# Optimization experiments

Hardware: AMD Instinct MI355X
Metric: run time of the kernel (lower is better)

## Reference

```python
import jax, jax.numpy as jnp
import numpy as np


def _component_indices(d, j):
    # Butterfly component at level j has block size k = d >> j.
    k = d >> j
    half = k // 2
    base = np.arange(d // k) * k                       # block starts
    p = (base[:, None] + np.arange(half)[None, :]).reshape(-1)  # [d//2]
    q = p + half
    return p, q


def butterfly_rotation(thetas, d):
    """Compose m = log2(d) butterfly components: R = B(d,d) @ B(d,d/2) @ ... @ B(d,2).
    thetas: [m, d//2] Givens angles per component (block-major order as in torch)."""
    m = thetas.shape[0]
    R = jnp.eye(d, dtype=thetas.dtype)
    for j in range(m):
        p, q = _component_indices(d, j)
        c = jnp.cos(thetas[j])
        s = jnp.sin(thetas[j])
        C = jnp.eye(d, dtype=thetas.dtype)
        C = C.at[p, p].set(c)
        C = C.at[q, q].set(c)
        C = C.at[p, q].set(-s)
        C = C.at[q, p].set(s)
        R = R @ C
    return R


def setup_inputs() -> dict:
    key = jax.random.key(0)
    ks = jax.random.split(key, 8)
    N, D_IN, D_OUT, R = 16384, 4096, 4096, 1024
    M = 10  # log2(R)
    return {
        "x": jax.random.normal(ks[0], (N, D_IN), dtype=jnp.float32),
        "W": jax.random.normal(ks[1], (D_OUT, D_IN), dtype=jnp.float32) * 0.02,
        "bias": jax.random.normal(ks[2], (D_OUT,), dtype=jnp.float32) * 0.02,
        "U": jax.random.normal(ks[3], (D_OUT, R), dtype=jnp.float32) * 0.02,
        "S": jax.random.uniform(ks[4], (R,), dtype=jnp.float32),
        "V": jax.random.normal(ks[5], (R, D_IN), dtype=jnp.float32) * 0.02,
        "thetas_u": jax.random.normal(ks[6], (M, R // 2), dtype=jnp.float32) * 0.1,
        "thetas_v": jax.random.normal(ks[7], (M, R // 2), dtype=jnp.float32) * 0.1,
    }


def reference(x, W, bias, U, S, V, thetas_u, thetas_v):
    r = S.shape[0]
    R_U = butterfly_rotation(thetas_u, r)  # [r, r]
    R_V = butterfly_rotation(thetas_v, r)  # [r, r]
    # base_layer(x)
    base = x @ W.T + bias                  # [N, out]
    # adapter: x @ V^T @ R_V @ diag(S) @ R_U^T @ U^T
    h = (x @ V.T) @ R_V                    # [N, r]
    h = h * S                              # diag(S)
    delta = (h @ R_U.T) @ U.T              # [N, out]
    return base + delta
```

## Files before the change

kernel.cpp:

```cpp
#include <hip/hip_runtime.h>
#include <cstdint>
#include <cstddef>


typedef __bf16 bf16x8 __attribute__((ext_vector_type(8)));
typedef float floatx4 __attribute__((ext_vector_type(4)));
typedef unsigned short ushortx8 __attribute__((ext_vector_type(8)));

__device__ __forceinline__ unsigned short f2bf(float f) {
    unsigned int u = __builtin_bit_cast(unsigned int, f);
    u += 0x7FFFu + ((u >> 16) & 1u);
    return (unsigned short)(u >> 16);
}

__device__ __forceinline__ void gld_lds16(const void* g, void* l) {
    __builtin_amdgcn_global_load_lds(
        (const __attribute__((address_space(1))) void*)g,
        (__attribute__((address_space(3))) void*)l,
        16, 0, 0);
}

__global__ __launch_bounds__(256) void butterfly_rows_kernel(
    const float* __restrict__ thetas_v, const float* __restrict__ thetas_u,
    const float* __restrict__ S,
    unsigned short* __restrict__ RVsb, unsigned short* __restrict__ RUb)
{
    const int d = 1024;
    __shared__ float w[1024];
    const int b   = blockIdx.x;
    const int mat = b >> 10;
    const int row = b & 1023;
    const float* th = mat ? thetas_u : thetas_v;
    const int t = threadIdx.x;

    for (int i = t; i < d; i += 256) w[i] = (i == row) ? 1.f : 0.f;
    __syncthreads();

    for (int j = 0; j < 10; ++j) {
        const int sh = 9 - j;
        const int halfm1 = (1 << sh) - 1;
        for (int i = t; i < d / 2; i += 256) {
            const int blk = i >> sh;
            const int off = i & halfm1;
            const int p = (blk << (sh + 1)) + off;
            const int q = p + (halfm1 + 1);
            const float theta = th[j * (d / 2) + i];
            float s, c;
            __sincosf(theta, &s, &c);
            const float wp = w[p], wq = w[q];
            w[p] = c * wp + s * wq;
            w[q] = -s * wp + c * wq;
        }
        __syncthreads();
    }

    if (mat == 0) {
        for (int i = t; i < d; i += 256) RVsb[row * d + i] = f2bf(w[i] * S[i]);
    } else {
        for (int i = t; i < d; i += 256) RUb[row * d + i] = f2bf(w[i]);
    }
}

__global__ __launch_bounds__(256) void cvt_f32_bf16_x8(
    const float* __restrict__ src, unsigned short* __restrict__ dst)
{
    const size_t i = ((size_t)blockIdx.x * 256 + threadIdx.x) * 8;
    float4 a = *(const float4*)(src + i);
    float4 b = *(const float4*)(src + i + 4);
    ushortx8 o;
    o[0] = f2bf(a.x); o[1] = f2bf(a.y); o[2] = f2bf(a.z); o[3] = f2bf(a.w);
    o[4] = f2bf(b.x); o[5] = f2bf(b.y); o[6] = f2bf(b.z); o[7] = f2bf(b.w);
    *(ushortx8*)(dst + i) = o;
}

__global__ __launch_bounds__(256) void transpose_to_bf16(
    const float* __restrict__ src, unsigned short* __restrict__ dst,
    int rows, int cols)
{
    __shared__ float tile[32][33];
    const int tx = threadIdx.x & 31, ty = threadIdx.x >> 5;
    const int c0 = blockIdx.x * 32, r0 = blockIdx.y * 32;
    for (int i = 0; i < 32; i += 8)
        tile[ty + i][tx] = src[(size_t)(r0 + ty + i) * cols + c0 + tx];
    __syncthreads();
    for (int i = 0; i < 32; i += 8)
        dst[(size_t)(c0 + ty + i) * rows + r0 + tx] = f2bf(tile[tx][ty + i]);
}

template <int EPI>
__global__ __launch_bounds__(256) void gemm_nt(
    const unsigned short* __restrict__ A,
    const unsigned short* __restrict__ B,
    float* __restrict__ Cf,
    unsigned short* __restrict__ Cb,
    const float* __restrict__ extra,
    int M, int N, int K)
{
    __shared__ __align__(16) unsigned short As[128 * 32];
    __shared__ __align__(16) unsigned short Bs[128 * 32];

    const int tid  = threadIdx.x;
    const int lane = tid & 63;
    const int wave = tid >> 6;
    const int wm = wave >> 1, wn = wave & 1;

    const int m0 = blockIdx.y * 128;
    const int n0 = blockIdx.x * 128;

    const int srow = wave * 32 + (lane >> 2);
    const int scol = (lane & 3) * 8;

    const unsigned short* gA = A + (size_t)(m0 + srow) * K + scol;
    const unsigned short* gB = B + (size_t)(n0 + srow) * K + scol;
    unsigned short* lA = As + wave * 32 * 32;
    unsigned short* lB = Bs + wave * 32 * 32;

    floatx4 acc[4][4];
#pragma unroll
    for (int i = 0; i < 4; ++i)
#pragma unroll
        for (int j = 0; j < 4; ++j) acc[i][j] = (floatx4)0.f;

    const int ar = lane & 15;
    const int ak = (lane >> 4) * 8;

    for (int kk = 0; kk < K; kk += 32) {
        gld_lds16(gA + kk, lA);
        gld_lds16(gA + kk + (size_t)16 * K, lA + 512);
        gld_lds16(gB + kk, lB);
        gld_lds16(gB + kk + (size_t)16 * K, lB + 512);
        __syncthreads();

        bf16x8 af[4], bfr[4];
#pragma unroll
        for (int tm = 0; tm < 4; ++tm)
            af[tm] = __builtin_bit_cast(bf16x8,
                *(const ushortx8*)&As[(wm * 64 + tm * 16 + ar) * 32 + ak]);
#pragma unroll
        for (int tn = 0; tn < 4; ++tn)
            bfr[tn] = __builtin_bit_cast(bf16x8,
                *(const ushortx8*)&Bs[(wn * 64 + tn * 16 + ar) * 32 + ak]);
#pragma unroll
        for (int tm = 0; tm < 4; ++tm)
#pragma unroll
            for (int tn = 0; tn < 4; ++tn)
                acc[tm][tn] = __builtin_amdgcn_mfma_f32_16x16x32_bf16(
                    af[tm], bfr[tn], acc[tm][tn], 0, 0, 0);
        __syncthreads();
    }

#pragma unroll
    for (int tm = 0; tm < 4; ++tm) {
#pragma unroll
        for (int tn = 0; tn < 4; ++tn) {
#pragma unroll
            for (int r = 0; r < 4; ++r) {
                const int row = m0 + wm * 64 + tm * 16 + (lane >> 4) * 4 + r;
                const int col = n0 + wn * 64 + tn * 16 + (lane & 15);
                const float v = acc[tm][tn][r];
                if (EPI == 1) {
                    Cf[(size_t)row * N + col] = v + extra[col];
                } else if (EPI == 2) {
                    Cb[(size_t)row * N + col] = f2bf(v);
                } else {
                    Cb[(size_t)row * N + col] = f2bf(v + extra[(size_t)row * N + col]);
                }
            }
        }
    }
}

extern "C" void kernel_launch(void* const* d_in, const int* in_sizes, int n_in,
                              void* d_out, int out_size, void* d_ws, size_t ws_size,
                              hipStream_t stream)
{
    const int NB = 16384, DIN = 4096, DOUT = 4096, R = 1024;

    const float* x    = (const float*)d_in[0];
    const float* W    = (const float*)d_in[1];
    const float* bias = (const float*)d_in[2];
    const float* U    = (const float*)d_in[3];
    const float* S    = (const float*)d_in[4];
    const float* V    = (const float*)d_in[5];
    const float* th_u = (const float*)d_in[6];
    const float* th_v = (const float*)d_in[7];
    float* out = (float*)d_out;

    char* ws = (char*)d_ws;
    size_t off = 0;
    auto alloc = [&](size_t bytes) {
        char* p = ws + off;
        off += (bytes + 255) & ~(size_t)255;
        return p;
    };
    unsigned short* Xb   = (unsigned short*)alloc((size_t)NB * DIN * 2);
    unsigned short* Wctb = (unsigned short*)alloc((size_t)DOUT * DIN * 2);
    unsigned short* RVsb = (unsigned short*)alloc((size_t)R * R * 2);
    unsigned short* RUb  = (unsigned short*)alloc((size_t)R * R * 2);
    unsigned short* Tb   = (unsigned short*)alloc((size_t)R * R * 2);
    unsigned short* Ub   = (unsigned short*)alloc((size_t)DOUT * R * 2);
    unsigned short* Gb   = (unsigned short*)alloc((size_t)DOUT * R * 2);
    unsigned short* Vtb  = (unsigned short*)alloc((size_t)DIN * R * 2);
    if (off > ws_size) return;

    butterfly_rows_kernel<<<2048, 256, 0, stream>>>(th_v, th_u, S, RVsb, RUb);

    cvt_f32_bf16_x8<<<(NB * (size_t)DIN) / 2048, 256, 0, stream>>>(x, Xb);
    cvt_f32_bf16_x8<<<((size_t)DOUT * R) / 2048, 256, 0, stream>>>(U, Ub);
    transpose_to_bf16<<<dim3(DIN / 32, R / 32), 256, 0, stream>>>(V, Vtb, R, DIN);

    gemm_nt<2><<<dim3(R / 128, R / 128), 256, 0, stream>>>(
        RVsb, RUb, nullptr, Tb, nullptr, R, R, R);

    gemm_nt<2><<<dim3(R / 128, DOUT / 128), 256, 0, stream>>>(
        Ub, Tb, nullptr, Gb, nullptr, DOUT, R, R);

    gemm_nt<3><<<dim3(DIN / 128, DOUT / 128), 256, 0, stream>>>(
        Gb, Vtb, nullptr, Wctb, W, DOUT, DIN, R);

    gemm_nt<1><<<dim3(DOUT / 128, NB / 128), 256, 0, stream>>>(
        Xb, Wctb, out, nullptr, bias, NB, DOUT, DIN);
}
```

Before: 1.312 ms.

## Add 256x256 double-buffered swizzled GEMM kernel for the large matmuls

Adds a new GEMM kernel with 256x256 tiles, 512 threads and K-step 64. It double-buffers direct global-to-LDS loads with explicit vmcnt waits, XOR-swizzles the LDS layout to avoid bank conflicts, raises wave priority around MFMA bursts, and optionally remaps workgroup IDs for L2 locality. The W-fold GEMM and the main x@W GEMM now use it, aiming at higher MFMA utilisation and less global and LDS traffic per flop. Costs are 128 KB of LDS per block, heavy register use from 32 accumulators, and a fixed tile-divisibility assumption.

```diff
diff --git a/kernel.cpp b/kernel.cpp
--- a/kernel.cpp
+++ b/kernel.cpp
@@ -168,6 +168,185 @@
             }
         }
     }
+}
+
+template <int EPI>
+__global__ __launch_bounds__(512, 2) void gemm256(
+    const unsigned short* __restrict__ A,
+    const unsigned short* __restrict__ B,
+    float* __restrict__ Cf,
+    unsigned short* __restrict__ Cb,
+    const float* __restrict__ extra,
+    int M, int N, int K, int swz_on)
+{
+    __shared__ __align__(16) unsigned short As[2][256 * 64];
+    __shared__ __align__(16) unsigned short Bs[2][256 * 64];
+
+    const int tid  = threadIdx.x;
+    const int lane = tid & 63;
+    const int wave = tid >> 6;
+    const int wm = wave >> 2;
+    const int wn = wave & 3;
+
+    int bx = blockIdx.x, by = blockIdx.y;
+    if (swz_on) {
+        const int gx  = gridDim.x;
+        const int nwg = gx * gridDim.y;
+        const int f   = by * gx + bx;
+        const int g   = (f & 7) * (nwg >> 3) + (f >> 3);
+        bx = g % gx;
+        by = g / gx;
+    }
+    const int m0 = by * 256;
+    const int n0 = bx * 256;
+
+    const int srow  = tid >> 3;
+    const int scolb = (tid & 7) << 4;
+    const int scol  = (scolb ^ ((srow & 7) << 4)) >> 1;
+
+    const unsigned short* gA = A + (size_t)(m0 + srow) * K + scol;
+    const unsigned short* gB = B + (size_t)(n0 + srow) * K + scol;
+    const int ldsoff = wave << 10;
+    const size_t rowstep = (size_t)64 * K;
+
+    const int fr   = lane & 15;
+    const int fk2  = ((lane >> 4) & 3) << 4;
+    const int swz  = (fr & 7) << 4;
+    const int ca0  = fk2 ^ swz;
+    const int ca1  = (64 + fk2) ^ swz;
+    const int arow = (wm * 128 + fr) << 7;
+    const int brow = (wn * 64 + fr) << 7;
+
+    floatx4 acc[8][4];
+#pragma unroll
+    for (int i = 0; i < 8; ++i)
+#pragma unroll
+        for (int j = 0; j < 4; ++j) acc[i][j] = (floatx4)0.f;
+
+    const int nkt = K >> 6;
+
+    {
+        char* la = (char*)&As[0][0] + ldsoff;
+        char* lb = (char*)&Bs[0][0] + ldsoff;
+#pragma unroll
+        for (int j = 0; j < 4; ++j) gld_lds16(gA + j * rowstep, la + j * 8192);
+#pragma unroll
+        for (int j = 0; j < 4; ++j) gld_lds16(gB + j * rowstep, lb + j * 8192);
+    }
+
+    for (int t = 0; t < nkt; ++t) {
+        if (t + 1 < nkt) {
+            const unsigned short* a = gA + (size_t)(t + 1) * 64;
+            const unsigned short* b = gB + (size_t)(t + 1) * 64;
+            char* la = (char*)&As[(t + 1) & 1][0] + ldsoff;
+            char* lb = (char*)&Bs[(t + 1) & 1][0] + ldsoff;
+#pragma unroll
+            for (int j = 0; j < 4; ++j) gld_lds16(a + j * rowstep, la + j * 8192);
+#pragma unroll
+            for (int j = 0; j < 4; ++j) gld_lds16(b + j * rowstep, lb + j * 8192);
+            __builtin_amdgcn_sched_barrier(0);
+            asm volatile("s_waitcnt vmcnt(8)" ::: "memory");
+        } else {
+            asm volatile("s_waitcnt vmcnt(0)" ::: "memory");
+        }
+        __builtin_amdgcn_s_barrier();
+        __builtin_amdgcn_sched_barrier(0);
+
+        const char* ab = (const char*)&As[t & 1][0];
+        const char* bb = (const char*)&Bs[t & 1][0];
+
+        bf16x8 af[4][2], b0[2][2], b1[2][2];
+
+#pragma unroll
+        for (int mf = 0; mf < 4; ++mf) {
+            af[mf][0] = __builtin_bit_cast(bf16x8, *(const ushortx8*)(ab + arow + (mf << 11) + ca0));
+            af[mf][1] = __builtin_bit_cast(bf16x8, *(const ushortx8*)(ab + arow + (mf << 11) + ca1));
+        }
+#pragma unroll
+        for (int nf = 0; nf < 2; ++nf) {
+            b0[nf][0] = __builtin_bit_cast(bf16x8, *(const ushortx8*)(bb + brow + (nf << 11) + ca0));
+            b0[nf][1] = __builtin_bit_cast(bf16x8, *(const ushortx8*)(bb + brow + (nf << 11) + ca1));
+        }
+        __builtin_amdgcn_s_setprio(1);
+#pragma unroll
+        for (int mf = 0; mf < 4; ++mf)
+#pragma unroll
+            for (int nf = 0; nf < 2; ++nf) {
+                acc[mf][nf] = __builtin_amdgcn_mfma_f32_16x16x32_bf16(af[mf][0], b0[nf][0], acc[mf][nf], 0, 0, 0);
+                acc[mf][nf] = __builtin_amdgcn_mfma_f32_16x16x32_bf16(af[mf][1], b0[nf][1], acc[mf][nf], 0, 0, 0);
+            }
+        __builtin_amdgcn_s_setprio(0);
+
+#pragma unroll
+        for (int nf = 0; nf < 2; ++nf) {
+            b1[nf][0] = __builtin_bit_cast(bf16x8, *(const ushortx8*)(bb + brow + 4096 + (nf << 11) + ca0));
+            b1[nf][1] = __builtin_bit_cast(bf16x8, *(const ushortx8*)(bb + brow + 4096 + (nf << 11) + ca1));
+        }
+        __builtin_amdgcn_s_setprio(1);
+#pragma unroll
+        for (int mf = 0; mf < 4; ++mf)
+#pragma unroll
+            for (int nf = 0; nf < 2; ++nf) {
+                acc[mf][2 + nf] = __builtin_amdgcn_mfma_f32_16x16x32_bf16(af[mf][0], b1[nf][0], acc[mf][2 + nf], 0, 0, 0);
+                acc[mf][2 + nf] = __builtin_amdgcn_mfma_f32_16x16x32_bf16(af[mf][1], b1[nf][1], acc[mf][2 + nf], 0, 0, 0);
+            }
+        __builtin_amdgcn_s_setprio(0);
+
+#pragma unroll
+        for (int mf = 0; mf < 4; ++mf) {
+            af[mf][0] = __builtin_bit_cast(bf16x8, *(const ushortx8*)(ab + arow + 8192 + (mf << 11) + ca0));
+            af[mf][1] = __builtin_bit_cast(bf16x8, *(const ushortx8*)(ab + arow + 8192 + (mf << 11) + ca1));
+        }
+        __builtin_amdgcn_s_setprio(1);
+#pragma unroll
+        for (int mf = 0; mf < 4; ++mf)
+#pragma unroll
+            for (int nf = 0; nf < 2; ++nf) {
+                acc[4 + mf][2 + nf] = __builtin_amdgcn_mfma_f32_16x16x32_bf16(af[mf][0], b1[nf][0], acc[4 + mf][2 + nf], 0, 0, 0);
+                acc[4 + mf][2 + nf] = __builtin_amdgcn_mfma_f32_16x16x32_bf16(af[mf][1], b1[nf][1], acc[4 + mf][2 + nf], 0, 0, 0);
+            }
+        __builtin_amdgcn_s_setprio(0);
+
+#pragma unroll
+        for (int nf = 0; nf < 2; ++nf) {
+            b0[nf][0] = __builtin_bit_cast(bf16x8, *(const ushortx8*)(bb + brow + (nf << 11) + ca0));
+            b0[nf][1] = __builtin_bit_cast(bf16x8, *(const ushortx8*)(bb + brow + (nf << 11) + ca1));
+        }
+        __builtin_amdgcn_s_setprio(1);
+#pragma unroll
+        for (int mf = 0; mf < 4; ++mf)
+#pragma unroll
+            for (int nf = 0; nf < 2; ++nf) {
+                acc[4 + mf][nf] = __builtin_amdgcn_mfma_f32_16x16x32_bf16(af[mf][0], b0[nf][0], acc[4 + mf][nf], 0, 0, 0);
+                acc[4 + mf][nf] = __builtin_amdgcn_mfma_f32_16x16x32_bf16(af[mf][1], b0[nf][1], acc[4 + mf][nf], 0, 0, 0);
+            }
+        __builtin_amdgcn_s_setprio(0);
+
+        __builtin_amdgcn_sched_barrier(0);
+        asm volatile("" ::: "memory");
+        __builtin_amdgcn_s_barrier();
+    }
+
+    const int er = wm * 128 + ((lane >> 4) << 2);
+    const int ec = wn * 64 + (lane & 15);
+#pragma unroll
+    for (int mfg = 0; mfg < 8; ++mfg) {
+#pragma unroll
+        for (int nfg = 0; nfg < 4; ++nfg) {
+#pragma unroll
+            for (int r = 0; r < 4; ++r) {
+                const int row = m0 + er + mfg * 16 + r;
+                const int col = n0 + ec + nfg * 16;
+                const float v = acc[mfg][nfg][r];
+                if (EPI == 1) {
+                    Cf[(size_t)row * N + col] = v + extra[col];
+                } else {
+                    Cb[(size_t)row * N + col] = f2bf(v + extra[(size_t)row * N + col]);
+                }
+            }
+        }
+    }
+    (void)M;
 }
 
 extern "C" void kernel_launch(void* const* d_in, const int* in_sizes, int n_in,
@@ -215,9 +394,9 @@
     gemm_nt<2><<<dim3(R / 128, DOUT / 128), 256, 0, stream>>>(
         Ub, Tb, nullptr, Gb, nullptr, DOUT, R, R);
 
-    gemm_nt<3><<<dim3(DIN / 128, DOUT / 128), 256, 0, stream>>>(
-        Gb, Vtb, nullptr, Wctb, W, DOUT, DIN, R);
-
-    gemm_nt<1><<<dim3(DOUT / 128, NB / 128), 256, 0, stream>>>(
-        Xb, Wctb, out, nullptr, bias, NB, DOUT, DIN);
-}
+    gemm256<3><<<dim3(DIN / 256, DOUT / 256), 512, 0, stream>>>(
+        Gb, Vtb, nullptr, Wctb, W, DOUT, DIN, R, 0);
+
+    gemm256<1><<<dim3(DOUT / 256, NB / 256), 512, 0, stream>>>(
+        Xb, Wctb, out, nullptr, bias, NB, DOUT, DIN, 1);
+}
```

After: 1.202 ms. 1.09x faster.
